# Optimization experiments

Measured on AMD Instinct MI355X. Metric: run time of the kernel, lower is better.

The kernel has to match this reference:

```python
import jax, jax.numpy as jnp
import numpy as np

B = 4194304   # batch of generated samples
C = 100       # number of classifier classes

def setup_inputs() -> dict:
    key = jax.random.key(0)
    logits = jax.random.normal(key, (B, C), dtype=jnp.float32)
    return {"logits": logits, "batch_size": B}

def reference(logits, batch_size):
    # argmax over classes -> predicted label per sample  [B]
    labels = jnp.argmax(logits, axis=1)
    # histogram of labels (replaces CPU Counter)          [C]
    counts = jnp.zeros((logits.shape[1],), dtype=jnp.float32).at[labels].add(1.0)
    p = counts / jnp.float32(batch_size)
    # entropy: -sum p*log2(p), skipping empty bins (Counter only iterates present labels)
    ent_terms = jnp.where(p > 0, p * (jnp.log(jnp.maximum(p, 1e-30)) / jnp.log(jnp.float32(2.0))), 0.0)
    loss = -jnp.sum(ent_terms)
    return loss
```

## Files before the change

kernel.cpp:

```cpp
#include <hip/hip_runtime.h>

#define NCLASS 100
#define TROWS 128
#define RSTRIDE 102

__global__ __launch_bounds__(128) void argmax_hist_kernel(
    const float4* __restrict__ g4,
    unsigned int* __restrict__ counts,
    int nrows)
{
    __shared__ float lds[TROWS * RSTRIDE];
    __shared__ unsigned int lhist[NCLASS];

    const int tid = threadIdx.x;
    for (int i = tid; i < NCLASS; i += TROWS) lhist[i] = 0u;
    __syncthreads();

    const int ntiles = nrows / TROWS;
    for (int tile = blockIdx.x; tile < ntiles; tile += gridDim.x) {
        const size_t base4 = (size_t)tile * (TROWS * 25);

        #pragma unroll
        for (int i = 0; i < 25; ++i) {
            const int f = i * TROWS + tid;
            float4 v = g4[base4 + f];
            const int r = f / 25;
            const int c = f - r * 25;
            float2* w = reinterpret_cast<float2*>(&lds[r * RSTRIDE + c * 4]);
            w[0] = make_float2(v.x, v.y);
            w[1] = make_float2(v.z, v.w);
        }
        __syncthreads();

        const float2* rp = reinterpret_cast<const float2*>(&lds[tid * RSTRIDE]);
        float best = -__builtin_huge_valf();
        int bidx = 0;
        #pragma unroll
        for (int j = 0; j < 50; ++j) {
            float2 v = rp[j];
            if (v.x > best) { best = v.x; bidx = 2 * j; }
            if (v.y > best) { best = v.y; bidx = 2 * j + 1; }
        }
        atomicAdd(&lhist[bidx], 1u);
        __syncthreads();
    }

    for (int i = tid; i < NCLASS; i += TROWS) {
        unsigned int c = lhist[i];
        if (c) atomicAdd(&counts[i], c);
    }
}

__global__ __launch_bounds__(128) void entropy_kernel(
    const unsigned int* __restrict__ counts,
    float* __restrict__ out,
    float invB)
{
    __shared__ float partial[128];
    const int t = threadIdx.x;
    float term = 0.0f;
    if (t < NCLASS) {
        float c = (float)counts[t];
        if (c > 0.0f) {
            float p = c * invB;
            term = p * (logf(p) * 1.4426950408889634f);
        }
    }
    partial[t] = term;
    __syncthreads();
    #pragma unroll
    for (int s = 64; s > 0; s >>= 1) {
        if (t < s) partial[t] += partial[t + s];
        __syncthreads();
    }
    if (t == 0) out[0] = -partial[0];
}

extern "C" void kernel_launch(void* const* d_in, const int* in_sizes, int n_in,
                              void* d_out, int out_size, void* d_ws, size_t ws_size,
                              hipStream_t stream)
{
    const float* logits = (const float*)d_in[0];
    const int nrows = in_sizes[0] / NCLASS;

    unsigned int* counts = (unsigned int*)d_ws;
    hipMemsetAsync(counts, 0, NCLASS * sizeof(unsigned int), stream);

    const int grid = 2048;
    argmax_hist_kernel<<<grid, TROWS, 0, stream>>>(
        (const float4*)logits, counts, nrows);

    entropy_kernel<<<1, 128, 0, stream>>>(counts, (float*)d_out, 1.0f / (float)nrows);
}
```

Baseline: 328.8 us.

## Prefetch next tile into registers with nontemporal loads, use 64-thread blocks

Software-pipelines the argmax kernel: each thread loads the next tile's logits into a 25-element register staging array while the current tile is written to LDS and reduced. Loads use nontemporal hints to avoid polluting caches with streaming data. Block size is halved to 64 rows and the grid doubled to 4096. The staging array raises register pressure, which may reduce occupancy.

Result: faster. 313.9 us (-4.6%).

```diff
diff --git a/kernel.cpp b/kernel.cpp
--- a/kernel.cpp
+++ b/kernel.cpp
@@ -1,11 +1,13 @@
 #include <hip/hip_runtime.h>
 
 #define NCLASS 100
-#define TROWS 128
+#define TROWS 64
 #define RSTRIDE 102
 
-__global__ __launch_bounds__(128) void argmax_hist_kernel(
-    const float4* __restrict__ g4,
+typedef float fx4 __attribute__((ext_vector_type(4)));
+
+__global__ __launch_bounds__(64) void argmax_hist_kernel(
+    const fx4* __restrict__ g4,
     unsigned int* __restrict__ counts,
     int nrows)
 {
@@ -13,23 +15,40 @@
     __shared__ unsigned int lhist[NCLASS];
 
     const int tid = threadIdx.x;
+    #pragma unroll
     for (int i = tid; i < NCLASS; i += TROWS) lhist[i] = 0u;
     __syncthreads();
 
     const int ntiles = nrows / TROWS;
-    for (int tile = blockIdx.x; tile < ntiles; tile += gridDim.x) {
-        const size_t base4 = (size_t)tile * (TROWS * 25);
+    fx4 stg[25];
 
+    int tile = blockIdx.x;
+    if (tile < ntiles) {
+        const size_t b4 = (size_t)tile * (TROWS * 25);
+        #pragma unroll
+        for (int i = 0; i < 25; ++i)
+            stg[i] = __builtin_nontemporal_load(&g4[b4 + i * TROWS + tid]);
+    }
+
+    while (tile < ntiles) {
         #pragma unroll
         for (int i = 0; i < 25; ++i) {
             const int f = i * TROWS + tid;
-            float4 v = g4[base4 + f];
             const int r = f / 25;
             const int c = f - r * 25;
             float2* w = reinterpret_cast<float2*>(&lds[r * RSTRIDE + c * 4]);
-            w[0] = make_float2(v.x, v.y);
-            w[1] = make_float2(v.z, v.w);
+            w[0] = make_float2(stg[i].x, stg[i].y);
+            w[1] = make_float2(stg[i].z, stg[i].w);
         }
+
+        const int ntile = tile + gridDim.x;
+        if (ntile < ntiles) {
+            const size_t b4 = (size_t)ntile * (TROWS * 25);
+            #pragma unroll
+            for (int i = 0; i < 25; ++i)
+                stg[i] = __builtin_nontemporal_load(&g4[b4 + i * TROWS + tid]);
+        }
+
         __syncthreads();
 
         const float2* rp = reinterpret_cast<const float2*>(&lds[tid * RSTRIDE]);
@@ -42,9 +61,12 @@
             if (v.y > best) { best = v.y; bidx = 2 * j + 1; }
         }
         atomicAdd(&lhist[bidx], 1u);
+
         __syncthreads();
+        tile = ntile;
     }
 
+    #pragma unroll
     for (int i = tid; i < NCLASS; i += TROWS) {
         unsigned int c = lhist[i];
         if (c) atomicAdd(&counts[i], c);
@@ -84,11 +106,11 @@
     const int nrows = in_sizes[0] / NCLASS;
 
     unsigned int* counts = (unsigned int*)d_ws;
-    hipMemsetAsync(counts, 0, NCLASS * sizeof(unsigned int), stream);
+    (void)hipMemsetAsync(counts, 0, NCLASS * sizeof(unsigned int), stream);
 
-    const int grid = 2048;
+    const int grid = 4096;
     argmax_hist_kernel<<<grid, TROWS, 0, stream>>>(
-        (const float4*)logits, counts, nrows);
+        (const fx4*)logits, counts, nrows);
 
     entropy_kernel<<<1, 128, 0, stream>>>(counts, (float*)d_out, 1.0f / (float)nrows);
 }
```
